# Performance work log

Measured on AMD Instinct MI355X. Metric: run time of the kernel, lower is better.

The kernel has to match this reference:

```python
import jax, jax.numpy as jnp
import numpy as np

E = 1024  # embedding_size
H = 16    # num_heads
D = E // H  # head_size = 64
SCALE = 1.0 / np.sqrt(np.float32(E))  # NOTE: original scales by sqrt(embedding_size), not head_size


def setup_inputs() -> dict:
    key = jax.random.key(0)
    ks = jax.random.split(key, 11)
    B, S = 2, 2048
    init = 1.0 / np.sqrt(np.float32(E))
    inp = {
        'q': jax.random.normal(ks[0], (B, S, E), dtype=jnp.float32),
        'k': jax.random.normal(ks[1], (B, S, E), dtype=jnp.float32),
        'v': jax.random.normal(ks[2], (B, S, E), dtype=jnp.float32),
        'wq': jax.random.normal(ks[3], (E, E), dtype=jnp.float32) * init,
        'bq': jax.random.normal(ks[4], (E,), dtype=jnp.float32) * init,
        'wk': jax.random.normal(ks[5], (E, E), dtype=jnp.float32) * init,
        'bk': jax.random.normal(ks[6], (E,), dtype=jnp.float32) * init,
        'wv': jax.random.normal(ks[7], (E, E), dtype=jnp.float32) * init,
        'bv': jax.random.normal(ks[8], (E,), dtype=jnp.float32) * init,
        'wo': jax.random.normal(ks[9], (E, E), dtype=jnp.float32) * init,
        'bo': jax.random.normal(ks[10], (E,), dtype=jnp.float32) * init,
    }
    return inp


def reference(q, k, v, wq, bq, wk, bk, wv, bv, wo, bo):
    S = q.shape[1]
    # Linear projections (torch Linear: x @ W.T + b)
    qp = (q @ wq.T + bq).reshape(-1, H, S, D)  # faithful raw view, not transpose
    kp = (k @ wk.T + bk).reshape(-1, H, S, D)
    vp = (v @ wv.T + bv).reshape(-1, H, S, D)
    # scores / sqrt(embedding_size) -- faithful to original (uses E, not D)
    scores = jnp.einsum('bhqd,bhkd->bhqk', qp, kp) * SCALE
    attn = jax.nn.softmax(scores, axis=-1)  # [B,H,S,S]
    out = jnp.einsum('bhqk,bhkd->bhqd', attn, vp)  # [B,H,S,D]
    out = out.reshape(-1, S, E)
    # dropout is eval-mode identity
    return out @ wo.T + bo
```

## Files before the change

kernel.cpp:

```cpp
#include <hip/hip_runtime.h>
#include <hip/hip_bf16.h>
#include <cstdint>


typedef __bf16 bf16_t;
typedef bf16_t bf16x8 __attribute__((ext_vector_type(8)));
typedef bf16_t bf16x4 __attribute__((ext_vector_type(4)));
typedef float  f32x4  __attribute__((ext_vector_type(4)));
typedef float  f32x16 __attribute__((ext_vector_type(16)));
typedef unsigned int u32;
typedef u32 u32x2 __attribute__((ext_vector_type(2)));

#define MFMA16(a, b, c) __builtin_amdgcn_mfma_f32_16x16x32_bf16((a), (b), (c), 0, 0, 0)
#define MFMA32(a, b, c) __builtin_amdgcn_mfma_f32_32x32x16_bf16((a), (b), (c), 0, 0, 0)

#define GLOAD_LDS16(gptr, lptr)                                                      \
  __builtin_amdgcn_global_load_lds(                                                  \
      (const __attribute__((address_space(1))) void*)(gptr),                         \
      (__attribute__((address_space(3))) void*)(lptr), 16, 0, 0)

namespace {
constexpr int kS = 2048, kE = 1024, kD = 64;
constexpr int kM = 4096;
constexpr float kQScaleL2E = 0.03125f * 1.44269504088896f;
}

__device__ inline u32 pkbf(float a, float b) {
  u32 r;
  asm("v_cvt_pk_bf16_f32 %0, %1, %2" : "=v"(r) : "v"(a), "v"(b));
  return r;
}

__device__ inline bf16x8 make_pfrag(float v0, float v1, float v2, float v3,
                                    float v4, float v5, float v6, float v7) {
  u32 A0 = pkbf(v0, v1), A1 = pkbf(v2, v3);
  u32 B0 = pkbf(v4, v5), B1 = pkbf(v6, v7);
  u32x2 r0 = __builtin_amdgcn_permlane32_swap(A0, B0, false, false);
  u32x2 r1 = __builtin_amdgcn_permlane32_swap(A1, B1, false, false);
  union { u32 w[4]; bf16x8 v; } u;
  u.w[0] = r0[0]; u.w[1] = r1[0]; u.w[2] = r0[1]; u.w[3] = r1[1];
  return u.v;
}

__device__ inline float xhalf_sum(float x) {
  u32 xu = __builtin_bit_cast(u32, x);
  u32x2 r = __builtin_amdgcn_permlane32_swap(xu, xu, false, false);
  return __builtin_bit_cast(float, r[0]) + __builtin_bit_cast(float, r[1]);
}

__global__ void cvt_batch(const float* __restrict__ s0, const float* __restrict__ s1,
                          const float* __restrict__ s2, const float* __restrict__ s3,
                          bf16_t* __restrict__ d0, bf16_t* __restrict__ d1,
                          bf16_t* __restrict__ d2, bf16_t* __restrict__ d3, int n4) {
  const float* s; bf16_t* d;
  switch (blockIdx.y) {
    case 0:  s = s0; d = d0; break;
    case 1:  s = s1; d = d1; break;
    case 2:  s = s2; d = d2; break;
    default: s = s3; d = d3; break;
  }
  int stride = gridDim.x * blockDim.x;
  for (int i = blockIdx.x * blockDim.x + threadIdx.x; i < n4; i += stride) {
    float4 v = reinterpret_cast<const float4*>(s)[i];
    bf16x4 o;
    o[0] = (bf16_t)v.x; o[1] = (bf16_t)v.y; o[2] = (bf16_t)v.z; o[3] = (bf16_t)v.w;
    reinterpret_cast<bf16x4*>(d)[i] = o;
  }
}

__global__ __launch_bounds__(256, 2)
void gemm_qkv(const bf16_t* __restrict__ qb, const bf16_t* __restrict__ kb,
              const bf16_t* __restrict__ vb, const bf16_t* __restrict__ W,
              const float* __restrict__ bq, const float* __restrict__ bk,
              const float* __restrict__ bv,
              bf16_t* __restrict__ Qp, bf16_t* __restrict__ Kp, bf16_t* __restrict__ Vp) {
  constexpr int K = kE, BK = 64;
  __shared__ __align__(16) bf16_t As[128 * BK];
  __shared__ __align__(16) bf16_t Bs[128 * BK];
  const int tid = threadIdx.x, lane = tid & 63, wave = tid >> 6;
  const int fr = lane & 15, fg = lane >> 4;
  const int region = blockIdx.x >> 3;
  const int bm = blockIdx.y * 128, bn = blockIdx.x * 128;
  const int bnl = (blockIdx.x & 7) * 128;
  const bf16_t* A = region == 0 ? qb : region == 1 ? kb : vb;
  const float* bias = region == 0 ? bq : region == 1 ? bk : bv;
  bf16_t* Cp = region == 0 ? Qp : region == 1 ? Kp : Vp;
  const float scale = region == 0 ? kQScaleL2E : 1.0f;
  const int wr = (wave >> 1) * 64, wc = (wave & 1) * 64;
  f32x4 acc[4][4] = {};
  for (int k0 = 0; k0 < K; k0 += BK) {
#pragma unroll
    for (int c = 0; c < 4; ++c) {
      int lin = c * 256 + tid, row = lin >> 3, ch = lin & 7, sch = ch ^ (row & 7);
      GLOAD_LDS16(A + (size_t)(bm + row) * K + k0 + sch * 8, (char*)As + lin * 16);
    }
#pragma unroll
    for (int c = 0; c < 4; ++c) {
      int lin = c * 256 + tid, row = lin >> 3, ch = lin & 7, sch = ch ^ (row & 7);
      GLOAD_LDS16(W + (size_t)(bn + row) * K + k0 + sch * 8, (char*)Bs + lin * 16);
    }
    __syncthreads();
#pragma unroll
    for (int kk = 0; kk < 2; ++kk) {
      bf16x8 af[4], bfv[4];
#pragma unroll
      for (int i = 0; i < 4; ++i) {
        int row = wr + i * 16 + fr;
        int ch = (kk * 4 + fg) ^ (row & 7);
        af[i] = *reinterpret_cast<const bf16x8*>((const char*)As + row * 128 + ch * 16);
      }
#pragma unroll
      for (int j = 0; j < 4; ++j) {
        int row = wc + j * 16 + fr;
        int ch = (kk * 4 + fg) ^ (row & 7);
        bfv[j] = *reinterpret_cast<const bf16x8*>((const char*)Bs + row * 128 + ch * 16);
      }
#pragma unroll
      for (int i = 0; i < 4; ++i)
#pragma unroll
        for (int j = 0; j < 4; ++j)
          acc[i][j] = MFMA16(af[i], bfv[j], acc[i][j]);
    }
    __syncthreads();
  }
#pragma unroll
  for (int i = 0; i < 4; ++i)
#pragma unroll
    for (int j = 0; j < 4; ++j) {
      int coll = bnl + wc + j * 16 + fr;
      float bvv = bias[coll];
#pragma unroll
      for (int r = 0; r < 4; ++r) {
        int row = bm + wr + i * 16 + fg * 4 + r;
        Cp[(size_t)row * kE + coll] = (bf16_t)((acc[i][j][r] + bvv) * scale);
      }
    }
}

__global__ __launch_bounds__(256, 2)
void gemm_out(const bf16_t* __restrict__ A, const bf16_t* __restrict__ Bm,
              const float* __restrict__ bias, float* __restrict__ Cout) {
  constexpr int K = kE, BK = 64;
  __shared__ __align__(16) bf16_t As[128 * BK];
  __shared__ __align__(16) bf16_t Bs[64 * BK];
  const int tid = threadIdx.x, lane = tid & 63, wave = tid >> 6;
  const int fr = lane & 15, fg = lane >> 4;
  const int bm = blockIdx.y * 128, bn = blockIdx.x * 64;
  const int wr = wave * 32;
  f32x4 acc[2][4] = {};
  for (int k0 = 0; k0 < K; k0 += BK) {
#pragma unroll
    for (int c = 0; c < 4; ++c) {
      int lin = c * 256 + tid, row = lin >> 3, ch = lin & 7, sch = ch ^ (row & 7);
      GLOAD_LDS16(A + (size_t)(bm + row) * K + k0 + sch * 8, (char*)As + lin * 16);
    }
#pragma unroll
    for (int c = 0; c < 2; ++c) {
      int lin = c * 256 + tid, row = lin >> 3, ch = lin & 7, sch = ch ^ (row & 7);
      GLOAD_LDS16(Bm + (size_t)(bn + row) * K + k0 + sch * 8, (char*)Bs + lin * 16);
    }
    __syncthreads();
#pragma unroll
    for (int kk = 0; kk < 2; ++kk) {
      bf16x8 af[2], bfv[4];
#pragma unroll
      for (int i = 0; i < 2; ++i) {
        int row = wr + i * 16 + fr;
        int ch = (kk * 4 + fg) ^ (row & 7);
        af[i] = *reinterpret_cast<const bf16x8*>((const char*)As + row * 128 + ch * 16);
      }
#pragma unroll
      for (int j = 0; j < 4; ++j) {
        int row = j * 16 + fr;
        int ch = (kk * 4 + fg) ^ (row & 7);
        bfv[j] = *reinterpret_cast<const bf16x8*>((const char*)Bs + row * 128 + ch * 16);
      }
#pragma unroll
      for (int i = 0; i < 2; ++i)
#pragma unroll
        for (int j = 0; j < 4; ++j)
          acc[i][j] = MFMA16(af[i], bfv[j], acc[i][j]);
    }
    __syncthreads();
  }
#pragma unroll
  for (int i = 0; i < 2; ++i)
#pragma unroll
    for (int j = 0; j < 4; ++j) {
      int col = bn + j * 16 + fr;
      float bvv = bias[col];
#pragma unroll
      for (int r = 0; r < 4; ++r) {
        int row = bm + wr + i * 16 + fg * 4 + r;
        Cout[(size_t)row * kE + col] = acc[i][j][r] + bvv;
      }
    }
}

__global__ __launch_bounds__(256)
void vtranspose(const bf16_t* __restrict__ Vp, bf16_t* __restrict__ VpT) {
  __shared__ __align__(16) bf16_t T[256 * 64];
  const int tid = threadIdx.x;
  const size_t hb = (size_t)blockIdx.y * (kS * kD);
  const bf16_t* src = Vp + hb + (size_t)blockIdx.x * 256 * kD;
  bf16_t* dst = VpT + hb + blockIdx.x * 256;
#pragma unroll
  for (int c = 0; c < 8; ++c) {
    int lin = c * 256 + tid;
    int row = lin >> 3, ch = lin & 7;
    bf16x8 v = *reinterpret_cast<const bf16x8*>(src + row * kD + ch * 8);
    *reinterpret_cast<bf16x8*>((char*)T + row * 128 + ((ch ^ ((row >> 3) & 7)) * 16)) = v;
  }
  __syncthreads();
#pragma unroll
  for (int c = 0; c < 8; ++c) {
    int lin = c * 256 + tid;
    int d = lin >> 5, kc = lin & 31;
    bf16x8 o;
#pragma unroll
    for (int e = 0; e < 8; ++e) {
      int s = kc * 8 + e;
      o[e] = *reinterpret_cast<const bf16_t*>(
          (const char*)T + s * 128 + (((d >> 3) ^ ((s >> 3) & 7)) * 16) + (d & 7) * 2);
    }
    *reinterpret_cast<bf16x8*>(dst + (size_t)d * kS + kc * 8) = o;
  }
}

__global__ __launch_bounds__(256, 2)
void attn_fwd(const bf16_t* __restrict__ Qp, const bf16_t* __restrict__ Kp,
              const bf16_t* __restrict__ VpT, bf16_t* __restrict__ Op) {
  __shared__ __align__(16) char smem[65536];
  const int tid = threadIdx.x, lane = tid & 63, wave = tid >> 6;
  const int ql = lane & 31, hi = lane >> 5;
  const int newb = ((int)blockIdx.x & 7) * 64 + ((int)blockIdx.x >> 3);
  const int head = newb >> 4, qt = newb & 15;
  const size_t hbase = (size_t)head * (kS * kD);
  const int q0 = qt * 128 + wave * 32;

  bf16x8 qf[4];
#pragma unroll
  for (int ct = 0; ct < 4; ++ct)
    qf[ct] = *reinterpret_cast<const bf16x8*>(
        Qp + hbase + (size_t)(q0 + ql) * kD + ct * 16 + hi * 8);

  float Lp = 0.0f;
  f32x16 o0 = {}, o1 = {};

  auto STAGE = [&](int kt, int b) {
    const bf16_t* Kt = Kp + hbase + (size_t)kt * 128 * kD;
    const bf16_t* Vt = VpT + hbase + kt * 128;
    char* Kd = smem + b * 32768;
    char* Vd = Kd + 16384;
#pragma unroll
    for (int c = 0; c < 4; ++c) {
      int lin = c * 256 + tid, row = lin >> 3, ch = lin & 7, sch = ch ^ (row & 7);
      GLOAD_LDS16(Kt + row * kD + sch * 8, Kd + lin * 16);
    }
#pragma unroll
    for (int c = 0; c < 4; ++c) {
      int lin = c * 256 + tid, row = lin >> 4, ch = lin & 15, sch = ch ^ (row & 15);
      GLOAD_LDS16(Vt + (size_t)row * kS + sch * 8, Vd + lin * 16);
    }
  };

  STAGE(0, 0);
#pragma unroll 1
  for (int kt = 0; kt < 16; ++kt) {
    __syncthreads();
    const char* Kb = smem + (kt & 1) * 32768;
    const char* Vb = Kb + 16384;
    if (kt + 1 < 16) STAGE(kt + 1, (kt + 1) & 1);

#pragma unroll
    for (int h = 0; h < 2; ++h) {
      f32x16 s0 = {}, s1 = {};
      __builtin_amdgcn_s_setprio(1);
#pragma unroll
      for (int ct = 0; ct < 4; ++ct) {
        const int r0 = h * 64 + ql, r1 = h * 64 + 32 + ql;
        bf16x8 k0 = *reinterpret_cast<const bf16x8*>(
            Kb + r0 * 128 + (((2 * ct + hi) ^ (r0 & 7)) * 16));
        bf16x8 k1 = *reinterpret_cast<const bf16x8*>(
            Kb + r1 * 128 + (((2 * ct + hi) ^ (r1 & 7)) * 16));
        s0 = MFMA32(k0, qf[ct], s0);
        s1 = MFMA32(k1, qf[ct], s1);
      }
      __builtin_amdgcn_s_setprio(0);

      float a0 = 0.f, a1 = 0.f;
#pragma unroll
      for (int r = 0; r < 16; ++r) {
        s0[r] = __builtin_amdgcn_exp2f(s0[r]);
        s1[r] = __builtin_amdgcn_exp2f(s1[r]);
        a0 += s0[r]; a1 += s1[r];
      }
      Lp += a0 + a1;

      bf16x8 pf0 = make_pfrag(s0[0], s0[1], s0[2], s0[3], s0[4], s0[5], s0[6], s0[7]);
      bf16x8 pf1 = make_pfrag(s0[8], s0[9], s0[10], s0[11], s0[12], s0[13], s0[14], s0[15]);
      bf16x8 pf2 = make_pfrag(s1[0], s1[1], s1[2], s1[3], s1[4], s1[5], s1[6], s1[7]);
      bf16x8 pf3 = make_pfrag(s1[8], s1[9], s1[10], s1[11], s1[12], s1[13], s1[14], s1[15]);

      __builtin_amdgcn_s_setprio(1);
#pragma unroll
      for (int j = 0; j < 4; ++j) {
        const int ks = h * 4 + j;
        const int r0 = ql, r1 = 32 + ql;
        bf16x8 v0 = *reinterpret_cast<const bf16x8*>(
            Vb + r0 * 256 + (((2 * ks + hi) ^ (r0 & 15)) * 16));
        bf16x8 v1 = *reinterpret_cast<const bf16x8*>(
            Vb + r1 * 256 + (((2 * ks + hi) ^ (r1 & 15)) * 16));
        bf16x8 pj = (j == 0) ? pf0 : (j == 1) ? pf1 : (j == 2) ? pf2 : pf3;
        o0 = MFMA32(v0, pj, o0);
        o1 = MFMA32(v1, pj, o1);
      }
      __builtin_amdgcn_s_setprio(0);
    }
  }

  float L = xhalf_sum(Lp);
  float inv = 1.0f / L;
#pragma unroll
  for (int r = 0; r < 16; ++r) { o0[r] *= inv; o1[r] *= inv; }
  __syncthreads();
  const int wb = wave * 4096;
#pragma unroll
  for (int c = 0; c < 4; ++c) {
    {
      u32 w0 = pkbf(o0[4 * c + 0], o0[4 * c + 1]);
      u32 w1 = pkbf(o0[4 * c + 2], o0[4 * c + 3]);
      int d0 = 8 * c + 4 * hi;
      int byte = (wb + ql * 128 + d0 * 2) ^ ((ql & 7) << 4);
      *reinterpret_cast<u32x2*>(smem + byte) = (u32x2){w0, w1};
    }
    {
      u32 w0 = pkbf(o1[4 * c + 0], o1[4 * c + 1]);
      u32 w1 = pkbf(o1[4 * c + 2], o1[4 * c + 3]);
      int d0 = 32 + 8 * c + 4 * hi;
      int byte = (wb + ql * 128 + d0 * 2) ^ ((ql & 7) << 4);
      *reinterpret_cast<u32x2*>(smem + byte) = (u32x2){w0, w1};
    }
  }
  asm volatile("s_waitcnt lgkmcnt(0)" ::: "memory");
  __builtin_amdgcn_sched_barrier(0);
#pragma unroll
  for (int it = 0; it < 4; ++it) {
    int lin = it * 64 + lane;
    int qr = lin >> 3, ch = lin & 7;
    int byte = wb + qr * 128 + ((ch * 16) ^ ((qr & 7) << 4));
    bf16x8 vrow = *reinterpret_cast<const bf16x8*>(smem + byte);
    *reinterpret_cast<bf16x8*>(Op + hbase + (size_t)(q0 + qr) * kD + ch * 8) = vrow;
  }
}

extern "C" void kernel_launch(void* const* d_in, const int* in_sizes, int n_in,
                              void* d_out, int out_size, void* d_ws, size_t ws_size,
                              hipStream_t stream) {
  (void)in_sizes; (void)n_in; (void)out_size; (void)ws_size;
  const float* q  = (const float*)d_in[0];
  const float* k  = (const float*)d_in[1];
  const float* v  = (const float*)d_in[2];
  const float* wq = (const float*)d_in[3];
  const float* bq = (const float*)d_in[4];
  const float* wk = (const float*)d_in[5];
  const float* bk = (const float*)d_in[6];
  const float* wv = (const float*)d_in[7];
  const float* bv = (const float*)d_in[8];
  const float* wo = (const float*)d_in[9];
  const float* bo = (const float*)d_in[10];
  float* out = (float*)d_out;

  char* ws = (char*)d_ws;
  const size_t MB = 1ull << 20;
  bf16_t* qb   = (bf16_t*)(ws +  0 * MB);
  bf16_t* kb   = (bf16_t*)(ws +  8 * MB);
  bf16_t* vb   = (bf16_t*)(ws + 16 * MB);
  bf16_t* wqkv = (bf16_t*)(ws + 24 * MB);
  bf16_t* wob  = (bf16_t*)(ws + 30 * MB);
  bf16_t* Qp   = (bf16_t*)(ws + 32 * MB);
  bf16_t* Kp   = (bf16_t*)(ws + 40 * MB);
  bf16_t* Vp   = (bf16_t*)(ws + 48 * MB);
  bf16_t* Opb  = (bf16_t*)(ws + 56 * MB);
  bf16_t* VpT  = (bf16_t*)(ws +  0 * MB);

  const int nQKV4 = (kM * kE) / 4;
  const int nW4 = (kE * kE) / 4;
  cvt_batch<<<dim3(512, 3), 256, 0, stream>>>(q, k, v, v, qb, kb, vb, vb, nQKV4);
  cvt_batch<<<dim3(128, 4), 256, 0, stream>>>(wq, wk, wv, wo, wqkv, wqkv + 1048576,
                                              wqkv + 2097152, wob, nW4);

  gemm_qkv<<<dim3(24, 32), 256, 0, stream>>>(qb, kb, vb, wqkv, bq, bk, bv, Qp, Kp, Vp);

  vtranspose<<<dim3(kS / 256, 32), 256, 0, stream>>>(Vp, VpT);

  attn_fwd<<<dim3(512), 256, 0, stream>>>(Qp, Kp, VpT, Opb);

  gemm_out<<<dim3(16, 32), 256, 0, stream>>>(Opb, wob, bo, out);
}
```

Before: 122.3 us.

## Split attention KV range across two wave groups and merge partial outputs

```diff
diff --git a/kernel.cpp b/kernel.cpp
--- a/kernel.cpp
+++ b/kernel.cpp
@@ -68,7 +68,7 @@
   }
 }
 
-__global__ __launch_bounds__(256, 2)
+__global__ __launch_bounds__(256, 3)
 void gemm_qkv(const bf16_t* __restrict__ qb, const bf16_t* __restrict__ kb,
               const bf16_t* __restrict__ vb, const bf16_t* __restrict__ W,
               const float* __restrict__ bq, const float* __restrict__ bk,
@@ -137,7 +137,7 @@
     }
 }
 
-__global__ __launch_bounds__(256, 2)
+__global__ __launch_bounds__(256, 3)
 void gemm_out(const bf16_t* __restrict__ A, const bf16_t* __restrict__ Bm,
               const float* __restrict__ bias, float* __restrict__ Cout) {
   constexpr int K = kE, BK = 64;
@@ -227,16 +227,21 @@
   }
 }
 
-__global__ __launch_bounds__(256, 2)
+__global__ __launch_bounds__(512, 4)
 void attn_fwd(const bf16_t* __restrict__ Qp, const bf16_t* __restrict__ Kp,
               const bf16_t* __restrict__ VpT, bf16_t* __restrict__ Op) {
-  __shared__ __align__(16) char smem[65536];
+  __shared__ __align__(16) char smem[66048];
   const int tid = threadIdx.x, lane = tid & 63, wave = tid >> 6;
   const int ql = lane & 31, hi = lane >> 5;
+  const int g = wave >> 2, ws = wave & 3;
+  const int tg = tid & 255;
   const int newb = ((int)blockIdx.x & 7) * 64 + ((int)blockIdx.x >> 3);
   const int head = newb >> 4, qt = newb & 15;
   const size_t hbase = (size_t)head * (kS * kD);
-  const int q0 = qt * 128 + wave * 32;
+  const int q0 = qt * 128 + ws * 32;
+  char* const gbase = smem + g * 32768;
+  const bf16_t* Kh = Kp + hbase + (size_t)(g * 1024) * kD;
+  const bf16_t* Vh = VpT + hbase + g * 1024;
 
   bf16x8 qf[4];
 #pragma unroll
@@ -247,110 +252,128 @@
   float Lp = 0.0f;
   f32x16 o0 = {}, o1 = {};
 
-  auto STAGE = [&](int kt, int b) {
-    const bf16_t* Kt = Kp + hbase + (size_t)kt * 128 * kD;
-    const bf16_t* Vt = VpT + hbase + kt * 128;
-    char* Kd = smem + b * 32768;
-    char* Vd = Kd + 16384;
-#pragma unroll
-    for (int c = 0; c < 4; ++c) {
-      int lin = c * 256 + tid, row = lin >> 3, ch = lin & 7, sch = ch ^ (row & 7);
+  auto STAGE = [&](int kt) {
+    const bf16_t* Kt = Kh + (size_t)kt * 64 * kD;
+    const bf16_t* Vt = Vh + kt * 64;
+    char* Kd = gbase + (kt & 1) * 16384;
+    char* Vd = Kd + 8192;
+#pragma unroll
+    for (int c = 0; c < 2; ++c) {
+      int lin = c * 256 + tg, row = lin >> 3, ch = lin & 7, sch = ch ^ (row & 7);
       GLOAD_LDS16(Kt + row * kD + sch * 8, Kd + lin * 16);
     }
 #pragma unroll
-    for (int c = 0; c < 4; ++c) {
-      int lin = c * 256 + tid, row = lin >> 4, ch = lin & 15, sch = ch ^ (row & 15);
+    for (int c = 0; c < 2; ++c) {
+      int lin = c * 256 + tg, row = lin >> 3, ch = lin & 7, sch = ch ^ (row & 7);
       GLOAD_LDS16(Vt + (size_t)row * kS + sch * 8, Vd + lin * 16);
     }
   };
 
-  STAGE(0, 0);
+  STAGE(0);
 #pragma unroll 1
   for (int kt = 0; kt < 16; ++kt) {
     __syncthreads();
-    const char* Kb = smem + (kt & 1) * 32768;
-    const char* Vb = Kb + 16384;
-    if (kt + 1 < 16) STAGE(kt + 1, (kt + 1) & 1);
-
-#pragma unroll
-    for (int h = 0; h < 2; ++h) {
-      f32x16 s0 = {}, s1 = {};
-      __builtin_amdgcn_s_setprio(1);
-#pragma unroll
-      for (int ct = 0; ct < 4; ++ct) {
-        const int r0 = h * 64 + ql, r1 = h * 64 + 32 + ql;
-        bf16x8 k0 = *reinterpret_cast<const bf16x8*>(
-            Kb + r0 * 128 + (((2 * ct + hi) ^ (r0 & 7)) * 16));
-        bf16x8 k1 = *reinterpret_cast<const bf16x8*>(
-            Kb + r1 * 128 + (((2 * ct + hi) ^ (r1 & 7)) * 16));
-        s0 = MFMA32(k0, qf[ct], s0);
-        s1 = MFMA32(k1, qf[ct], s1);
-      }
-      __builtin_amdgcn_s_setprio(0);
-
-      float a0 = 0.f, a1 = 0.f;
-#pragma unroll
-      for (int r = 0; r < 16; ++r) {
-        s0[r] = __builtin_amdgcn_exp2f(s0[r]);
-        s1[r] = __builtin_amdgcn_exp2f(s1[r]);
-        a0 += s0[r]; a1 += s1[r];
-      }
-      Lp += a0 + a1;
-
-      bf16x8 pf0 = make_pfrag(s0[0], s0[1], s0[2], s0[3], s0[4], s0[5], s0[6], s0[7]);
-      bf16x8 pf1 = make_pfrag(s0[8], s0[9], s0[10], s0[11], s0[12], s0[13], s0[14], s0[15]);
-      bf16x8 pf2 = make_pfrag(s1[0], s1[1], s1[2], s1[3], s1[4], s1[5], s1[6], s1[7]);
-      bf16x8 pf3 = make_pfrag(s1[8], s1[9], s1[10], s1[11], s1[12], s1[13], s1[14], s1[15]);
-
-      __builtin_amdgcn_s_setprio(1);
-#pragma unroll
-      for (int j = 0; j < 4; ++j) {
-        const int ks = h * 4 + j;
-        const int r0 = ql, r1 = 32 + ql;
-        bf16x8 v0 = *reinterpret_cast<const bf16x8*>(
-            Vb + r0 * 256 + (((2 * ks + hi) ^ (r0 & 15)) * 16));
-        bf16x8 v1 = *reinterpret_cast<const bf16x8*>(
-            Vb + r1 * 256 + (((2 * ks + hi) ^ (r1 & 15)) * 16));
-        bf16x8 pj = (j == 0) ? pf0 : (j == 1) ? pf1 : (j == 2) ? pf2 : pf3;
-        o0 = MFMA32(v0, pj, o0);
-        o1 = MFMA32(v1, pj, o1);
-      }
-      __builtin_amdgcn_s_setprio(0);
-    }
-  }
-
-  float L = xhalf_sum(Lp);
-  float inv = 1.0f / L;
-#pragma unroll
-  for (int r = 0; r < 16; ++r) { o0[r] *= inv; o1[r] *= inv; }
+    const char* Kb = gbase + (kt & 1) * 16384;
+    const char* Vb = Kb + 8192;
+    if (kt + 1 < 16) STAGE(kt + 1);
+
+    f32x16 s0 = {}, s1 = {};
+    __builtin_amdgcn_s_setprio(1);
+#pragma unroll
+    for (int ct = 0; ct < 4; ++ct) {
+      bf16x8 k0 = *reinterpret_cast<const bf16x8*>(
+          Kb + ql * 128 + (((2 * ct + hi) ^ (ql & 7)) * 16));
+      bf16x8 k1 = *reinterpret_cast<const bf16x8*>(
+          Kb + (32 + ql) * 128 + (((2 * ct + hi) ^ (ql & 7)) * 16));
+      s0 = MFMA32(k0, qf[ct], s0);
+      s1 = MFMA32(k1, qf[ct], s1);
+    }
+    __builtin_amdgcn_s_setprio(0);
+
+    float a0 = 0.f, a1 = 0.f;
+#pragma unroll
+    for (int r = 0; r < 16; ++r) {
+      s0[r] = __builtin_amdgcn_exp2f(s0[r]);
+      s1[r] = __builtin_amdgcn_exp2f(s1[r]);
+      a0 += s0[r]; a1 += s1[r];
+    }
+    Lp += a0 + a1;
+
+    bf16x8 pf0 = make_pfrag(s0[0], s0[1], s0[2], s0[3], s0[4], s0[5], s0[6], s0[7]);
+    bf16x8 pf1 = make_pfrag(s0[8], s0[9], s0[10], s0[11], s0[12], s0[13], s0[14], s0[15]);
+    bf16x8 pf2 = make_pfrag(s1[0], s1[1], s1[2], s1[3], s1[4], s1[5], s1[6], s1[7]);
+    bf16x8 pf3 = make_pfrag(s1[8], s1[9], s1[10], s1[11], s1[12], s1[13], s1[14], s1[15]);
+
+    __builtin_amdgcn_s_setprio(1);
+#pragma unroll
+    for (int j = 0; j < 4; ++j) {
+      bf16x8 v0 = *reinterpret_cast<const bf16x8*>(
+          Vb + ql * 128 + (((2 * j + hi) ^ (ql & 7)) * 16));
+      bf16x8 v1 = *reinterpret_cast<const bf16x8*>(
+          Vb + (32 + ql) * 128 + (((2 * j + hi) ^ (ql & 7)) * 16));
+      bf16x8 pj = (j == 0) ? pf0 : (j == 1) ? pf1 : (j == 2) ? pf2 : pf3;
+      o0 = MFMA32(v0, pj, o0);
+      o1 = MFMA32(v1, pj, o1);
+    }
+    __builtin_amdgcn_s_setprio(0);
+  }
+
   __syncthreads();
-  const int wb = wave * 4096;
-#pragma unroll
-  for (int c = 0; c < 4; ++c) {
-    {
-      u32 w0 = pkbf(o0[4 * c + 0], o0[4 * c + 1]);
-      u32 w1 = pkbf(o0[4 * c + 2], o0[4 * c + 3]);
-      int d0 = 8 * c + 4 * hi;
-      int byte = (wb + ql * 128 + d0 * 2) ^ ((ql & 7) << 4);
-      *reinterpret_cast<u32x2*>(smem + byte) = (u32x2){w0, w1};
-    }
-    {
-      u32 w0 = pkbf(o1[4 * c + 0], o1[4 * c + 1]);
-      u32 w1 = pkbf(o1[4 * c + 2], o1[4 * c + 3]);
-      int d0 = 32 + 8 * c + 4 * hi;
-      int byte = (wb + ql * 128 + d0 * 2) ^ ((ql & 7) << 4);
-      *reinterpret_cast<u32x2*>(smem + byte) = (u32x2){w0, w1};
-    }
-  }
-  asm volatile("s_waitcnt lgkmcnt(0)" ::: "memory");
-  __builtin_amdgcn_sched_barrier(0);
-#pragma unroll
-  for (int it = 0; it < 4; ++it) {
-    int lin = it * 64 + lane;
-    int qr = lin >> 3, ch = lin & 7;
-    int byte = wb + qr * 128 + ((ch * 16) ^ ((qr & 7) << 4));
-    bf16x8 vrow = *reinterpret_cast<const bf16x8*>(smem + byte);
-    *reinterpret_cast<bf16x8*>(Op + hbase + (size_t)(q0 + qr) * kD + ch * 8) = vrow;
+  if (g == 1) {
+    char* pb = smem + 32768 + ws * 8192;
+#pragma unroll
+    for (int c = 0; c < 4; ++c) {
+      *reinterpret_cast<f32x4*>(pb + c * 1024 + lane * 16) =
+          (f32x4){o0[4 * c], o0[4 * c + 1], o0[4 * c + 2], o0[4 * c + 3]};
+      *reinterpret_cast<f32x4*>(pb + 4096 + c * 1024 + lane * 16) =
+          (f32x4){o1[4 * c], o1[4 * c + 1], o1[4 * c + 2], o1[4 * c + 3]};
+    }
+    float Lb = xhalf_sum(Lp);
+    if (hi == 0) *reinterpret_cast<float*>(smem + 65536 + (ws * 32 + ql) * 4) = Lb;
+  }
+  __syncthreads();
+  if (g == 0) {
+    const char* pb = smem + 32768 + ws * 8192;
+#pragma unroll
+    for (int c = 0; c < 4; ++c) {
+      f32x4 r0 = *reinterpret_cast<const f32x4*>(pb + c * 1024 + lane * 16);
+      f32x4 r1 = *reinterpret_cast<const f32x4*>(pb + 4096 + c * 1024 + lane * 16);
+#pragma unroll
+      for (int i = 0; i < 4; ++i) { o0[4 * c + i] += r0[i]; o1[4 * c + i] += r1[i]; }
+    }
+    float L = xhalf_sum(Lp) +
+              *reinterpret_cast<const float*>(smem + 65536 + (ws * 32 + ql) * 4);
+    float inv = 1.0f / L;
+#pragma unroll
+    for (int r = 0; r < 16; ++r) { o0[r] *= inv; o1[r] *= inv; }
+    const int wb = ws * 4096;
+#pragma unroll
+    for (int c = 0; c < 4; ++c) {
+      {
+        u32 w0 = pkbf(o0[4 * c + 0], o0[4 * c + 1]);
+        u32 w1 = pkbf(o0[4 * c + 2], o0[4 * c + 3]);
+        int d0 = 8 * c + 4 * hi;
+        int byte = (wb + ql * 128 + d0 * 2) ^ ((ql & 7) << 4);
+        *reinterpret_cast<u32x2*>(smem + byte) = (u32x2){w0, w1};
+      }
+      {
+        u32 w0 = pkbf(o1[4 * c + 0], o1[4 * c + 1]);
+        u32 w1 = pkbf(o1[4 * c + 2], o1[4 * c + 3]);
+        int d0 = 32 + 8 * c + 4 * hi;
+        int byte = (wb + ql * 128 + d0 * 2) ^ ((ql & 7) << 4);
+        *reinterpret_cast<u32x2*>(smem + byte) = (u32x2){w0, w1};
+      }
+    }
+    asm volatile("s_waitcnt lgkmcnt(0)" ::: "memory");
+    __builtin_amdgcn_sched_barrier(0);
+#pragma unroll
+    for (int it = 0; it < 4; ++it) {
+      int lin = it * 64 + lane;
+      int qr = lin >> 3, ch = lin & 7;
+      int byte = wb + qr * 128 + ((ch * 16) ^ ((qr & 7) << 4));
+      bf16x8 vrow = *reinterpret_cast<const bf16x8*>(smem + byte);
+      *reinterpret_cast<bf16x8*>(Op + hbase + (size_t)(q0 + qr) * kD + ch * 8) = vrow;
+    }
   }
 }
 
@@ -394,7 +417,7 @@
 
   vtranspose<<<dim3(kS / 256, 32), 256, 0, stream>>>(Vp, VpT);
 
-  attn_fwd<<<dim3(512), 256, 0, stream>>>(Qp, Kp, VpT, Opb);
+  attn_fwd<<<dim3(512), 512, 0, stream>>>(Qp, Kp, VpT, Opb);
 
   gemm_out<<<dim3(16, 32), 256, 0, stream>>>(Opb, wob, bo, out);
 }
```

Measured after the change: 120.6 us. About the same (-1.4%).
